# Optimization experiments

Hardware: AMD Instinct MI355X
Metric: run time of the kernel (lower is better)

## Reference

```python
import jax, jax.numpy as jnp
import numpy as np

EPS = float(np.finfo(np.float64).eps)  # np.finfo(float).eps as in torch combine


def setup_inputs() -> dict:
    key = jax.random.key(0)
    ks = jax.random.split(key, 4)
    B, E, D_in, D_h, D_out = 4096, 8, 768, 2048, 768
    return {
        "x": jax.random.normal(ks[0], (B, D_in), dtype=jnp.float32),
        "w_gate": jax.random.normal(ks[1], (D_in, E), dtype=jnp.float32) * 0.02,
        "W1": jax.random.normal(ks[2], (E, D_in, D_h), dtype=jnp.float32) * (1.0 / np.sqrt(D_in)),
        "b1": jnp.zeros((E, D_h), dtype=jnp.float32),
        "W2": jax.random.normal(ks[3], (E, D_h, D_out), dtype=jnp.float32) * (1.0 / np.sqrt(D_h)),
        "b2": jnp.zeros((E, D_out), dtype=jnp.float32),
        "k": 2,
    }


def _cv_squared(v):
    # torch .var() is unbiased (ddof=1)
    return jnp.var(v, ddof=1) / (jnp.mean(v) ** 2 + 1e-10)


def _top_k_gates(logits, k):
    B, E = logits.shape
    top_vals, top_idx = jax.lax.top_k(logits, k)        # [B, k]
    top_gates = jax.nn.softmax(top_vals, axis=1)        # softmax over the k kept logits
    gates = jnp.zeros((B, E), logits.dtype).at[jnp.arange(B)[:, None], top_idx].set(top_gates)
    return gates


def reference(x, w_gate, W1, b1, W2, b2, k):
    # --- gating (eval path: noiseless clean logits, softmax gating) ---
    logits = x @ w_gate                                  # [B, E]
    gates = _top_k_gates(logits, k)                      # [B, E], sparse (k nonzeros/row)
    # --- per-expert MLP: Linear -> gelu -> Linear -> log_softmax ---
    # Dense grouped compute over experts; gate==0 terms contribute nothing in combine.
    h = jax.nn.gelu(jnp.einsum('bi,eih->beh', x, W1) + b1[None])      # [B, E, Dh]
    lo = jax.nn.log_softmax(jnp.einsum('beh,eho->beo', h, W2) + b2[None], axis=-1)  # [B, E, Do]
    # --- combine: exp, weight by gates, scatter-add, eps-clamp, log ---
    combined = jnp.einsum('be,beo->bo', gates, jnp.exp(lo))           # [B, Do]
    y = jnp.log(jnp.where(combined == 0, EPS, combined))
    # --- load-balancing aux loss (eval: load = count of nonzero gates) ---
    importance = gates.sum(0)
    load = (gates > 0).sum(0).astype(jnp.float32)
    loss = 0.01 * (_cv_squared(importance) + _cv_squared(load))
    return y, loss
```

## Files before the change

kernel.cpp:

```cpp
#include <hip/hip_runtime.h>
#include <hip/hip_bf16.h>
#include <math.h>

typedef __hip_bfloat16 bf16;
typedef short v8s __attribute__((ext_vector_type(8)));
typedef float v4f __attribute__((ext_vector_type(4)));

#define B_TOK 4096
#define E_EXP 8
#define D_IN  768
#define D_H   2048
#define D_OUT 768
#define MAXT  72

__device__ __forceinline__ void gl_lds16(const bf16* g, bf16* l) {
  __builtin_amdgcn_global_load_lds(
      (const __attribute__((address_space(1))) unsigned int*)g,
      (__attribute__((address_space(3))) unsigned int*)l, 16, 0, 0);
}

__device__ __forceinline__ void transpose_tile64(
    const float* __restrict__ W, bf16* __restrict__ Wt,
    int K, int N, int e, int k0, int n0, int t, bf16 (*tile)[72]) {
  const int w = t >> 6, l = t & 63;
  const float* Wp = W + (size_t)e * K * N;
  #pragma unroll
  for (int p = 0; p < 4; ++p) {
    int k_loc = w * 16 + p * 4 + (l >> 4);
    int nn = (l & 15) * 4;
    float4 v = *(const float4*)(Wp + (size_t)(k0 + k_loc) * N + n0 + nn);
    float vv[4] = {v.x, v.y, v.z, v.w};
    #pragma unroll
    for (int i = 0; i < 4; ++i) {
      int n_loc = nn + i;
      int phys = (k_loc >> 3) ^ ((n_loc >> 2) & 7);
      tile[n_loc][phys * 8 + (k_loc & 7)] = __float2bfloat16(vv[i]);
    }
  }
  __syncthreads();
  bf16* Wtp = Wt + (size_t)e * N * K;
  const int nsub = l >> 2;
  #pragma unroll
  for (int p2 = 0; p2 < 2; ++p2) {
    int c = (l & 3) + p2 * 4;
    int n_loc = w * 16 + nsub;
    int phys = c ^ ((n_loc >> 2) & 7);
    v8s val = *(const v8s*)&tile[n_loc][phys * 8];
    *(v8s*)(Wtp + (size_t)(n0 + n_loc) * K + k0 + c * 8) = val;
  }
}

__global__ __launch_bounds__(256)
void prep_kernel(const float* __restrict__ x, const float* __restrict__ wg,
                 const float* __restrict__ W1, bf16* __restrict__ W1t,
                 bf16* __restrict__ xb, float* __restrict__ gates,
                 int* __restrict__ tidx) {
  __shared__ bf16 tile[64][72];
  const int b = blockIdx.x;
  const int t = threadIdx.x;
  if (b < 3072) {
    int e = b / 384, rem = b % 384;
    int kb = rem % 12, nb = rem / 12;
    transpose_tile64(W1, W1t, D_IN, D_H, e, kb * 64, nb * 64, t, tile);
  } else {
    int gt = (b - 3072) * 256 + t;
    int tok = gt >> 6, l = gt & 63;
    const float* xr = x + (size_t)tok * D_IN;
    bf16* xbr = xb + (size_t)tok * D_IN;
    float acc[8] = {0.f,0.f,0.f,0.f,0.f,0.f,0.f,0.f};
    #pragma unroll
    for (int i = 0; i < 3; ++i) {
      int k0 = i * 256 + l * 4;
      float4 v = *(const float4*)(xr + k0);
      union { bf16 h[4]; uint2 u; } pk;
      pk.h[0] = __float2bfloat16(v.x); pk.h[1] = __float2bfloat16(v.y);
      pk.h[2] = __float2bfloat16(v.z); pk.h[3] = __float2bfloat16(v.w);
      *(uint2*)(xbr + k0) = pk.u;
      float xv[4] = {v.x, v.y, v.z, v.w};
      #pragma unroll
      for (int j = 0; j < 4; ++j) {
        const float* wr = wg + (size_t)(k0 + j) * 8;
        float4 w0 = *(const float4*)wr;
        float4 w1 = *(const float4*)(wr + 4);
        acc[0] += xv[j] * w0.x; acc[1] += xv[j] * w0.y;
        acc[2] += xv[j] * w0.z; acc[3] += xv[j] * w0.w;
        acc[4] += xv[j] * w1.x; acc[5] += xv[j] * w1.y;
        acc[6] += xv[j] * w1.z; acc[7] += xv[j] * w1.w;
      }
    }
    #pragma unroll
    for (int d = 1; d < 64; d <<= 1)
      #pragma unroll
      for (int e2 = 0; e2 < 8; ++e2) acc[e2] += __shfl_xor(acc[e2], d);
    if (l == 0) {
      int i1 = 0; float v1 = acc[0];
      #pragma unroll
      for (int e2 = 1; e2 < 8; ++e2) if (acc[e2] > v1) { v1 = acc[e2]; i1 = e2; }
      int i2 = -1; float v2 = -1e30f;
      #pragma unroll
      for (int e2 = 0; e2 < 8; ++e2) if (e2 != i1 && acc[e2] > v2) { v2 = acc[e2]; i2 = e2; }
      float ex = __expf(v2 - v1);
      float g1 = 1.f / (1.f + ex), g2 = ex / (1.f + ex);
      gates[2 * tok] = g1; gates[2 * tok + 1] = g2;
      tidx[2 * tok] = i1;  tidx[2 * tok + 1] = i2;
    }
  }
}

__global__ void finalize_kernel(const int* __restrict__ tidx, const float* __restrict__ gates,
                                int* __restrict__ cnt_off, int* __restrict__ row_ids,
                                int* __restrict__ pos, int* __restrict__ tmap,
                                float* __restrict__ loss_out) {
  __shared__ int   hcnt[256][9];
  __shared__ float himp[256][9];
  __shared__ int   tot[8], off[8];
  __shared__ float itot[8];
  int t = threadIdx.x;
  #pragma unroll
  for (int e = 0; e < 8; ++e) { hcnt[t][e] = 0; himp[t][e] = 0.f; }
  __syncthreads();
  for (int i = 0; i < 32; ++i) {
    int idx = t * 32 + i;
    int e = tidx[idx];
    hcnt[t][e] += 1;
    himp[t][e] += gates[idx];
  }
  __syncthreads();
  if (t < 8) {
    int run = 0; float s = 0.f;
    for (int j = 0; j < 256; ++j) {
      int c = hcnt[j][t];
      hcnt[j][t] = run;
      run += c;
      s += himp[j][t];
    }
    tot[t] = run; itot[t] = s;
  }
  __syncthreads();
  if (t == 0) {
    int o = 0;
    float mi = 0.f, ml = 0.f;
    for (int e = 0; e < 8; ++e) {
      off[e] = o; o += tot[e];
      cnt_off[e] = tot[e]; cnt_off[8 + e] = off[e];
      mi += itot[e]; ml += (float)tot[e];
    }
    mi *= 0.125f; ml *= 0.125f;
    float vi = 0.f, vl = 0.f;
    for (int e = 0; e < 8; ++e) {
      float d = itot[e] - mi;        vi += d * d;
      float d2 = (float)tot[e] - ml; vl += d2 * d2;
    }
    vi /= 7.f; vl /= 7.f;
    *loss_out = 0.01f * (vi / (mi * mi + 1e-10f) + vl / (ml * ml + 1e-10f));
    int nt = 0;
    for (int e = 0; e < 8; ++e)
      for (int tt = 0; tt < (tot[e] + 127) >> 7; ++tt) {
        tmap[nt] = e; tmap[MAXT + nt] = tt; ++nt;
      }
    for (; nt < MAXT; ++nt) tmap[nt] = -1;
  }
  __syncthreads();
  for (int i = 0; i < 32; ++i) {
    int idx = t * 32 + i;
    int e = tidx[idx];
    int slot = off[e] + hcnt[t][e];
    hcnt[t][e] += 1;
    row_ids[slot] = idx >> 1;
    pos[idx] = slot;
  }
}

template<int KDIM, bool GATHER, bool GELU, bool DOTRANS>
__global__ __launch_bounds__(256, 2)
void gemm_bn256(const bf16* __restrict__ Ab, const bf16* __restrict__ Wt,
                const float* __restrict__ bias, bf16* __restrict__ Outb,
                const int* __restrict__ row_ids, const int* __restrict__ cnt_off,
                const int* __restrict__ tmap, const int N,
                const float* __restrict__ Wsrc, bf16* __restrict__ Wdst) {
  constexpr int BK = 32, BM = 128, BN = 256;
  constexpr int NK = KDIM / BK;
  static_assert(NK % 2 == 0 && NK >= 4, "NK even, >=4");
  __shared__ __align__(16) bf16 lds[2][(BM + BN) * BK];
  const int t = (int)threadIdx.x, w = t >> 6, l = t & 63;
  if (DOTRANS && blockIdx.y >= MAXT) {
    int tid = (blockIdx.y - MAXT) * gridDim.x + blockIdx.x;
    int e = tid / 96, r = tid % 96;
    int kb = r % 8, nb = r / 8;
    bf16 (*tile)[72] = (bf16(*)[72])&lds[0][0];
    #pragma unroll 1
    for (int sub = 0; sub < 4; ++sub) {
      transpose_tile64(Wsrc, Wdst, D_H, D_OUT, e, kb * 256 + sub * 64, nb * 64, t, tile);
      __syncthreads();
    }
    return;
  }
  const int ti = blockIdx.y;
  const int e = tmap[ti];
  if (e < 0) return;
  const int rowb = tmap[MAXT + ti];
  const int cnt = cnt_off[e];
  const int off = cnt_off[8 + e];
  const int colb = blockIdx.x;
  const int cs = (l & 3) ^ ((l >> 3) & 3);
  const bf16* gA[2];
  const bf16* gB[4];
  #pragma unroll
  for (int it = 0; it < 2; ++it) {
    int rt = (it * 4 + w) * 16 + (l >> 2);
    int r = rowb * BM + rt;
    int rc = r < cnt ? r : cnt - 1;
    long arow = GATHER ? (long)row_ids[off + rc] : (long)(off + rc);
    gA[it] = Ab + arow * (long)KDIM + cs * 8;
  }
  #pragma unroll
  for (int it = 0; it < 4; ++it) {
    int rt = (it * 4 + w) * 16 + (l >> 2);
    gB[it] = Wt + ((size_t)e * N + (size_t)colb * BN + rt) * KDIM + cs * 8;
  }
  v4f acc[4][8] = {};
  const int wm = w >> 1, wn = w & 1;

#define STAGE(b, k0) do {                                                   \
    _Pragma("unroll")                                                       \
    for (int it = 0; it < 2; ++it)                                          \
      gl_lds16(gA[it] + (k0), &lds[b][(it * 4 + w) * 512]);                 \
    _Pragma("unroll")                                                       \
    for (int it = 0; it < 4; ++it)                                          \
      gl_lds16(gB[it] + (k0), &lds[b][BM * BK + (it * 4 + w) * 512]);       \
  } while (0)

#define COMPUTE(b) do {                                                     \
    __builtin_amdgcn_s_setprio(1);                                          \
    v8s af[4], bfr[8];                                                      \
    const int p = (l >> 4) ^ ((l >> 1) & 3);                                \
    _Pragma("unroll")                                                       \
    for (int fm = 0; fm < 4; ++fm) {                                        \
      int row = wm * 64 + fm * 16 + (l & 15);                               \
      af[fm] = *(const v8s*)(&lds[b][0] + row * BK + p * 8);                \
    }                                                                       \
    _Pragma("unroll")                                                       \
    for (int fn = 0; fn < 8; ++fn) {                                        \
      int row = wn * 128 + fn * 16 + (l & 15);                              \
      bfr[fn] = *(const v8s*)(&lds[b][BM * BK] + row * BK + p * 8);         \
    }                                                                       \
    _Pragma("unroll")                                                       \
    for (int fm = 0; fm < 4; ++fm)                                          \
      _Pragma("unroll")                                                     \
      for (int fn = 0; fn < 8; ++fn)                                        \
        acc[fm][fn] = __builtin_amdgcn_mfma_f32_16x16x32_bf16(af[fm], bfr[fn], acc[fm][fn], 0, 0, 0); \
    __builtin_amdgcn_s_setprio(0);                                          \
  } while (0)

#define SB    __builtin_amdgcn_sched_barrier(0)
#define BARR  __builtin_amdgcn_s_barrier()
#define WAIT6 asm volatile("s_waitcnt vmcnt(6)" ::: "memory")
#define WAITZ asm volatile("s_waitcnt vmcnt(0)" ::: "memory")

  STAGE(0, 0);
  #pragma unroll 1
  for (int ks = 0; ks < NK - 2; ks += 2) {
    STAGE(1, (ks + 1) * BK);
    WAIT6; SB; BARR; SB;
    COMPUTE(0);
    BARR; SB;
    STAGE(0, (ks + 2) * BK);
    WAIT6; SB; BARR; SB;
    COMPUTE(1);
    BARR; SB;
  }
  STAGE(1, (NK - 1) * BK);
  WAIT6; SB; BARR; SB;
  COMPUTE(0);
  WAITZ; SB; BARR; SB;
  COMPUTE(1);
  BARR; SB;
#undef STAGE
#undef COMPUTE
#undef WAIT6
#undef WAITZ

  float* eps = (float*)(&lds[0][0]) + w * (16 * 132);
  const float* bpp = bias + (size_t)e * N + (size_t)colb * BN + wn * 128;
  float bv[2][8];
  #pragma unroll
  for (int pp = 0; pp < 2; ++pp)
    #pragma unroll
    for (int jj = 0; jj < 8; ++jj) bv[pp][jj] = bpp[pp * 64 + (l & 7) * 8 + jj];
  #pragma unroll
  for (int fm = 0; fm < 4; ++fm) {
    #pragma unroll
    for (int fn = 0; fn < 8; ++fn)
      #pragma unroll
      for (int q = 0; q < 4; ++q)
        eps[((l >> 4) * 4 + q) * 132 + fn * 16 + (l & 15)] = acc[fm][fn][q];
    #pragma unroll
    for (int half = 0; half < 2; ++half) {
      int row = (l >> 3) + 8 * half;
      int r = rowb * BM + wm * 64 + fm * 16 + row;
      if (r < cnt) {
        #pragma unroll
        for (int pp = 0; pp < 2; ++pp) {
          const float* rp = eps + row * 132 + pp * 64 + (l & 7) * 8;
          union { bf16 h[8]; uint4 u; } pk;
          #pragma unroll
          for (int jj = 0; jj < 8; ++jj) {
            float v = rp[jj] + bv[pp][jj];
            if (GELU) {
              float u = 0.7978845608028654f * (v + 0.044715f * v * v * v);
              float th = 1.f - 2.f / (__expf(2.f * u) + 1.f);
              v = 0.5f * v * (1.f + th);
            }
            pk.h[jj] = __float2bfloat16(v);
          }
          *(uint4*)(Outb + (size_t)(off + r) * N + (size_t)colb * BN
                    + wn * 128 + pp * 64 + (l & 7) * 8) = pk.u;
        }
      }
    }
  }
#undef SB
#undef BARR
}

template<int KDIM, bool GELU>
__global__ __launch_bounds__(256, 4)
void gemm_bk32(const bf16* __restrict__ Ab, const bf16* __restrict__ Wt,
               const float* __restrict__ bias, bf16* __restrict__ Outb,
               const int* __restrict__ cnt_off, const int* __restrict__ tmap,
               const int N) {
  constexpr int BK = 32, BM = 128, BN = 128;
  constexpr int NK = KDIM / BK;
  static_assert(NK % 2 == 0 && NK >= 4, "NK even, >=4");
  __shared__ __align__(16) bf16 lds[2][(BM + BN) * BK];
  const int t = (int)threadIdx.x, w = t >> 6, l = t & 63;
  const int ti = blockIdx.y;
  const int e = tmap[ti];
  if (e < 0) return;
  const int rowb = tmap[MAXT + ti];
  const int cnt = cnt_off[e];
  const int off = cnt_off[8 + e];
  const int colb = blockIdx.x;
  const int cs = (l & 3) ^ ((l >> 3) & 3);
  const bf16* gA[2];
  const bf16* gB[2];
  #pragma unroll
  for (int it = 0; it < 2; ++it) {
    int rt = (it * 4 + w) * 16 + (l >> 2);
    int r = rowb * BM + rt;
    int rc = r < cnt ? r : cnt - 1;
    gA[it] = Ab + (long)(off + rc) * KDIM + cs * 8;
    gB[it] = Wt + ((size_t)e * N + (size_t)colb * BN + rt) * KDIM + cs * 8;
  }
  v4f acc[4][4] = {};
  const int wm = w >> 1, wn = w & 1;

#define STAGE(b, k0) do {                                                   \
    _Pragma("unroll")                                                       \
    for (int it = 0; it < 2; ++it)                                          \
      gl_lds16(gA[it] + (k0), &lds[b][(it * 4 + w) * 512]);                 \
    _Pragma("unroll")                                                       \
    for (int it = 0; it < 2; ++it)                                          \
      gl_lds16(gB[it] + (k0), &lds[b][BM * BK + (it * 4 + w) * 512]);       \
  } while (0)

#define COMPUTE(b) do {                                                     \
    __builtin_amdgcn_s_setprio(1);                                          \
    v8s af[4], bfr[4];                                                      \
    const int p = (l >> 4) ^ ((l >> 1) & 3);                                \
    _Pragma("unroll")                                                       \
    for (int fm = 0; fm < 4; ++fm) {                                        \
      int row = wm * 64 + fm * 16 + (l & 15);                               \
      af[fm] = *(const v8s*)(&lds[b][0] + row * BK + p * 8);                \
    }                                                                       \
    _Pragma("unroll")                                                       \
    for (int fn = 0; fn < 4; ++fn) {                                        \
      int row = wn * 64 + fn * 16 + (l & 15);                               \
      bfr[fn] = *(const v8s*)(&lds[b][BM * BK] + row * BK + p * 8);         \
    }                                                                       \
    _Pragma("unroll")                                                       \
    for (int fm = 0; fm < 4; ++fm)                                          \
      _Pragma("unroll")                                                     \
      for (int fn = 0; fn < 4; ++fn)                                        \
        acc[fm][fn] = __builtin_amdgcn_mfma_f32_16x16x32_bf16(af[fm], bfr[fn], acc[fm][fn], 0, 0, 0); \
    __builtin_amdgcn_s_setprio(0);                                          \
  } while (0)

#define SB    __builtin_amdgcn_sched_barrier(0)
#define BARR  __builtin_amdgcn_s_barrier()
#define WAIT4 asm volatile("s_waitcnt vmcnt(4)" ::: "memory")
#define WAITZ asm volatile("s_waitcnt vmcnt(0)" ::: "memory")

  STAGE(0, 0);
  #pragma unroll 1
  for (int ks = 0; ks < NK - 2; ks += 2) {
    STAGE(1, (ks + 1) * BK);
    WAIT4; SB; BARR; SB;
    COMPUTE(0);
    BARR; SB;
    STAGE(0, (ks + 2) * BK);
    WAIT4; SB; BARR; SB;
    COMPUTE(1);
    BARR; SB;
  }
  STAGE(1, (NK - 1) * BK);
  WAIT4; SB; BARR; SB;
  COMPUTE(0);
  WAITZ; SB; BARR; SB;
  COMPUTE(1);
  BARR; SB;
#undef STAGE
#undef COMPUTE
#undef WAIT4
#undef WAITZ

  float* eps = (float*)(&lds[0][0]) + w * (16 * 68);
  const float* bp = bias + (size_t)e * N + (size_t)colb * BN + wn * 64 + (l & 7) * 8;
  float bv[8];
  #pragma unroll
  for (int jj = 0; jj < 8; ++jj) bv[jj] = bp[jj];
  #pragma unroll
  for (int fm = 0; fm < 4; ++fm) {
    #pragma unroll
    for (int fn = 0; fn < 4; ++fn)
      #pragma unroll
      for (int q = 0; q < 4; ++q)
        eps[((l >> 4) * 4 + q) * 68 + fn * 16 + (l & 15)] = acc[fm][fn][q];
    #pragma unroll
    for (int half = 0; half < 2; ++half) {
      int row = (l >> 3) + 8 * half;
      int r = rowb * BM + wm * 64 + fm * 16 + row;
      if (r < cnt) {
        const float* rp = eps + row * 68 + (l & 7) * 8;
        union { bf16 h[8]; uint4 u; } pk;
        #pragma unroll
        for (int jj = 0; jj < 8; ++jj) {
          float v = rp[jj] + bv[jj];
          if (GELU) {
            float u = 0.7978845608028654f * (v + 0.044715f * v * v * v);
            float th = 1.f - 2.f / (__expf(2.f * u) + 1.f);
            v = 0.5f * v * (1.f + th);
          }
          pk.h[jj] = __float2bfloat16(v);
        }
        *(uint4*)(Outb + (size_t)(off + r) * N + (size_t)colb * BN + wn * 64 + (l & 7) * 8) = pk.u;
      }
    }
  }
#undef SB
#undef BARR
}

__global__ void combine_kernel(const bf16* __restrict__ z, const float* __restrict__ gates,
                               const int* __restrict__ pos, float* __restrict__ y) {
  int gt = blockIdx.x * 256 + threadIdx.x;
  int tok = gt >> 6, l = gt & 63;
  if (tok >= B_TOK) return;
  const ushort4* z1 = (const ushort4*)(z + (size_t)pos[2 * tok] * D_OUT);
  const ushort4* z2 = (const ushort4*)(z + (size_t)pos[2 * tok + 1] * D_OUT);
  float g1 = gates[2 * tok], g2 = gates[2 * tok + 1];
  float a[12], b[12];
  float m1 = -1e30f, m2 = -1e30f;
  #pragma unroll
  for (int i = 0; i < 3; ++i) {
    ushort4 u1 = z1[l + i * 64];
    ushort4 u2 = z2[l + i * 64];
    unsigned s1v[4] = {u1.x, u1.y, u1.z, u1.w};
    unsigned s2v[4] = {u2.x, u2.y, u2.z, u2.w};
    #pragma unroll
    for (int j = 0; j < 4; ++j) {
      union { unsigned u; float f; } c1, c2;
      c1.u = s1v[j] << 16; c2.u = s2v[j] << 16;
      a[i * 4 + j] = c1.f; b[i * 4 + j] = c2.f;
      m1 = fmaxf(m1, c1.f); m2 = fmaxf(m2, c2.f);
    }
  }
  #pragma unroll
  for (int d = 1; d < 64; d <<= 1) {
    m1 = fmaxf(m1, __shfl_xor(m1, d));
    m2 = fmaxf(m2, __shfl_xor(m2, d));
  }
  float s1 = 0.f, s2 = 0.f;
  #pragma unroll
  for (int i = 0; i < 12; ++i) { s1 += __expf(a[i] - m1); s2 += __expf(b[i] - m2); }
  #pragma unroll
  for (int d = 1; d < 64; d <<= 1) { s1 += __shfl_xor(s1, d); s2 += __shfl_xor(s2, d); }
  float c1 = g1 / s1, c2 = g2 / s2;
  float4* yo = (float4*)(y + (size_t)tok * D_OUT);
  #pragma unroll
  for (int i = 0; i < 3; ++i) {
    float4 o;
    float* op = (float*)&o;
    #pragma unroll
    for (int j = 0; j < 4; ++j) {
      float cmb = c1 * __expf(a[i * 4 + j] - m1) + c2 * __expf(b[i * 4 + j] - m2);
      op[j] = logf(cmb == 0.f ? 2.2204460492503131e-16f : cmb);
    }
    yo[l + i * 64] = o;
  }
}

extern "C" void kernel_launch(void* const* d_in, const int* in_sizes, int n_in,
                              void* d_out, int out_size, void* d_ws, size_t ws_size,
                              hipStream_t stream) {
  const float* x  = (const float*)d_in[0];
  const float* wg = (const float*)d_in[1];
  const float* W1 = (const float*)d_in[2];
  const float* b1 = (const float*)d_in[3];
  const float* W2 = (const float*)d_in[4];
  const float* b2 = (const float*)d_in[5];
  float* out = (float*)d_out;

  char* ws = (char*)d_ws;
  int*   cnt_off = (int*)(ws + 0);
  float* gates   = (float*)(ws + 256);
  int*   tidx    = (int*)(ws + 256 + 32768);
  int*   pos     = (int*)(ws + 256 + 65536);
  int*   row_ids = (int*)(ws + 256 + 98304);
  int*   tmap    = (int*)(ws + 256 + 131072);
  const size_t base = 262144;
  bf16* x_bf = (bf16*)(ws + base);
  bf16* W1t  = (bf16*)(ws + base + 6291456);
  bf16* W2t  = (bf16*)(ws + base + 31457280);
  bf16* h_bf = (bf16*)(ws + base + 56623104);
  bf16* z_bf = (bf16*)(ws + base);

  prep_kernel<<<dim3(4096), 256, 0, stream>>>(x, wg, W1, W1t, x_bf, gates, tidx);
  finalize_kernel<<<dim3(1), 256, 0, stream>>>(tidx, gates, cnt_off, row_ids, pos, tmap,
                                               out + (size_t)B_TOK * D_OUT);
  gemm_bn256<D_IN, true, true, true><<<dim3(D_H / 256, MAXT + 96), 256, 0, stream>>>(
      x_bf, W1t, b1, h_bf, row_ids, cnt_off, tmap, D_H, W2, W2t);
  gemm_bk32<D_H, false><<<dim3(D_OUT / 128, MAXT), 256, 0, stream>>>(
      h_bf, W2t, b2, z_bf, cnt_off, tmap, D_OUT);
  combine_kernel<<<dim3(1024), 256, 0, stream>>>(z_bf, gates, pos, out);
}
```

Baseline: 162.9 us.

## Shrink first GEMM tile to BN=128; load second GEMM weights directly to registers

The first expert GEMM (fused with the gather, GELU and W2 transpose) now uses 128x128 tiles with higher occupancy instead of 128x256 tiles. The transpose work is spread over the new grid shape. The second GEMM gets a new kernel that stages only the activation tile through LDS and loads weight fragments straight from global memory into registers, double-buffered alongside the LDS stage. This aims to cut LDS traffic and footprint and raise occupancy, at the risk of less coalesced global reads of weights and less weight reuse across waves.

```diff
diff --git a/kernel.cpp b/kernel.cpp
--- a/kernel.cpp
+++ b/kernel.cpp
@@ -172,13 +172,13 @@
 }
 
 template<int KDIM, bool GATHER, bool GELU, bool DOTRANS>
-__global__ __launch_bounds__(256, 2)
-void gemm_bn256(const bf16* __restrict__ Ab, const bf16* __restrict__ Wt,
-                const float* __restrict__ bias, bf16* __restrict__ Outb,
-                const int* __restrict__ row_ids, const int* __restrict__ cnt_off,
-                const int* __restrict__ tmap, const int N,
-                const float* __restrict__ Wsrc, bf16* __restrict__ Wdst) {
-  constexpr int BK = 32, BM = 128, BN = 256;
+__global__ __launch_bounds__(256, 4)
+void gemm_bk32(const bf16* __restrict__ Ab, const bf16* __restrict__ Wt,
+               const float* __restrict__ bias, bf16* __restrict__ Outb,
+               const int* __restrict__ row_ids, const int* __restrict__ cnt_off,
+               const int* __restrict__ tmap, const int N,
+               const float* __restrict__ Wsrc, bf16* __restrict__ Wdst) {
+  constexpr int BK = 32, BM = 128, BN = 128;
   constexpr int NK = KDIM / BK;
   static_assert(NK % 2 == 0 && NK >= 4, "NK even, >=4");
   __shared__ __align__(16) bf16 lds[2][(BM + BN) * BK];
@@ -204,7 +204,7 @@
   const int colb = blockIdx.x;
   const int cs = (l & 3) ^ ((l >> 3) & 3);
   const bf16* gA[2];
-  const bf16* gB[4];
+  const bf16* gB[2];
   #pragma unroll
   for (int it = 0; it < 2; ++it) {
     int rt = (it * 4 + w) * 16 + (l >> 2);
@@ -212,144 +212,6 @@
     int rc = r < cnt ? r : cnt - 1;
     long arow = GATHER ? (long)row_ids[off + rc] : (long)(off + rc);
     gA[it] = Ab + arow * (long)KDIM + cs * 8;
-  }
-  #pragma unroll
-  for (int it = 0; it < 4; ++it) {
-    int rt = (it * 4 + w) * 16 + (l >> 2);
-    gB[it] = Wt + ((size_t)e * N + (size_t)colb * BN + rt) * KDIM + cs * 8;
-  }
-  v4f acc[4][8] = {};
-  const int wm = w >> 1, wn = w & 1;
-
-#define STAGE(b, k0) do {                                                   \
-    _Pragma("unroll")                                                       \
-    for (int it = 0; it < 2; ++it)                                          \
-      gl_lds16(gA[it] + (k0), &lds[b][(it * 4 + w) * 512]);                 \
-    _Pragma("unroll")                                                       \
-    for (int it = 0; it < 4; ++it)                                          \
-      gl_lds16(gB[it] + (k0), &lds[b][BM * BK + (it * 4 + w) * 512]);       \
-  } while (0)
-
-#define COMPUTE(b) do {                                                     \
-    __builtin_amdgcn_s_setprio(1);                                          \
-    v8s af[4], bfr[8];                                                      \
-    const int p = (l >> 4) ^ ((l >> 1) & 3);                                \
-    _Pragma("unroll")                                                       \
-    for (int fm = 0; fm < 4; ++fm) {                                        \
-      int row = wm * 64 + fm * 16 + (l & 15);                               \
-      af[fm] = *(const v8s*)(&lds[b][0] + row * BK + p * 8);                \
-    }                                                                       \
-    _Pragma("unroll")                                                       \
-    for (int fn = 0; fn < 8; ++fn) {                                        \
-      int row = wn * 128 + fn * 16 + (l & 15);                              \
-      bfr[fn] = *(const v8s*)(&lds[b][BM * BK] + row * BK + p * 8);         \
-    }                                                                       \
-    _Pragma("unroll")                                                       \
-    for (int fm = 0; fm < 4; ++fm)                                          \
-      _Pragma("unroll")                                                     \
-      for (int fn = 0; fn < 8; ++fn)                                        \
-        acc[fm][fn] = __builtin_amdgcn_mfma_f32_16x16x32_bf16(af[fm], bfr[fn], acc[fm][fn], 0, 0, 0); \
-    __builtin_amdgcn_s_setprio(0);                                          \
-  } while (0)
-
-#define SB    __builtin_amdgcn_sched_barrier(0)
-#define BARR  __builtin_amdgcn_s_barrier()
-#define WAIT6 asm volatile("s_waitcnt vmcnt(6)" ::: "memory")
-#define WAITZ asm volatile("s_waitcnt vmcnt(0)" ::: "memory")
-
-  STAGE(0, 0);
-  #pragma unroll 1
-  for (int ks = 0; ks < NK - 2; ks += 2) {
-    STAGE(1, (ks + 1) * BK);
-    WAIT6; SB; BARR; SB;
-    COMPUTE(0);
-    BARR; SB;
-    STAGE(0, (ks + 2) * BK);
-    WAIT6; SB; BARR; SB;
-    COMPUTE(1);
-    BARR; SB;
-  }
-  STAGE(1, (NK - 1) * BK);
-  WAIT6; SB; BARR; SB;
-  COMPUTE(0);
-  WAITZ; SB; BARR; SB;
-  COMPUTE(1);
-  BARR; SB;
-#undef STAGE
-#undef COMPUTE
-#undef WAIT6
-#undef WAITZ
-
-  float* eps = (float*)(&lds[0][0]) + w * (16 * 132);
-  const float* bpp = bias + (size_t)e * N + (size_t)colb * BN + wn * 128;
-  float bv[2][8];
-  #pragma unroll
-  for (int pp = 0; pp < 2; ++pp)
-    #pragma unroll
-    for (int jj = 0; jj < 8; ++jj) bv[pp][jj] = bpp[pp * 64 + (l & 7) * 8 + jj];
-  #pragma unroll
-  for (int fm = 0; fm < 4; ++fm) {
-    #pragma unroll
-    for (int fn = 0; fn < 8; ++fn)
-      #pragma unroll
-      for (int q = 0; q < 4; ++q)
-        eps[((l >> 4) * 4 + q) * 132 + fn * 16 + (l & 15)] = acc[fm][fn][q];
-    #pragma unroll
-    for (int half = 0; half < 2; ++half) {
-      int row = (l >> 3) + 8 * half;
-      int r = rowb * BM + wm * 64 + fm * 16 + row;
-      if (r < cnt) {
-        #pragma unroll
-        for (int pp = 0; pp < 2; ++pp) {
-          const float* rp = eps + row * 132 + pp * 64 + (l & 7) * 8;
-          union { bf16 h[8]; uint4 u; } pk;
-          #pragma unroll
-          for (int jj = 0; jj < 8; ++jj) {
-            float v = rp[jj] + bv[pp][jj];
-            if (GELU) {
-              float u = 0.7978845608028654f * (v + 0.044715f * v * v * v);
-              float th = 1.f - 2.f / (__expf(2.f * u) + 1.f);
-              v = 0.5f * v * (1.f + th);
-            }
-            pk.h[jj] = __float2bfloat16(v);
-          }
-          *(uint4*)(Outb + (size_t)(off + r) * N + (size_t)colb * BN
-                    + wn * 128 + pp * 64 + (l & 7) * 8) = pk.u;
-        }
-      }
-    }
-  }
-#undef SB
-#undef BARR
-}
-
-template<int KDIM, bool GELU>
-__global__ __launch_bounds__(256, 4)
-void gemm_bk32(const bf16* __restrict__ Ab, const bf16* __restrict__ Wt,
-               const float* __restrict__ bias, bf16* __restrict__ Outb,
-               const int* __restrict__ cnt_off, const int* __restrict__ tmap,
-               const int N) {
-  constexpr int BK = 32, BM = 128, BN = 128;
-  constexpr int NK = KDIM / BK;
-  static_assert(NK % 2 == 0 && NK >= 4, "NK even, >=4");
-  __shared__ __align__(16) bf16 lds[2][(BM + BN) * BK];
-  const int t = (int)threadIdx.x, w = t >> 6, l = t & 63;
-  const int ti = blockIdx.y;
-  const int e = tmap[ti];
-  if (e < 0) return;
-  const int rowb = tmap[MAXT + ti];
-  const int cnt = cnt_off[e];
-  const int off = cnt_off[8 + e];
-  const int colb = blockIdx.x;
-  const int cs = (l & 3) ^ ((l >> 3) & 3);
-  const bf16* gA[2];
-  const bf16* gB[2];
-  #pragma unroll
-  for (int it = 0; it < 2; ++it) {
-    int rt = (it * 4 + w) * 16 + (l >> 2);
-    int r = rowb * BM + rt;
-    int rc = r < cnt ? r : cnt - 1;
-    gA[it] = Ab + (long)(off + rc) * KDIM + cs * 8;
     gB[it] = Wt + ((size_t)e * N + (size_t)colb * BN + rt) * KDIM + cs * 8;
   }
   v4f acc[4][4] = {};
@@ -451,6 +313,141 @@
 #undef BARR
 }
 
+template<int KDIM, bool GELU>
+__global__ __launch_bounds__(256, 3)
+void gemm_directb(const bf16* __restrict__ Ab, const bf16* __restrict__ Wt,
+                  const float* __restrict__ bias, bf16* __restrict__ Outb,
+                  const int* __restrict__ cnt_off, const int* __restrict__ tmap,
+                  const int N) {
+  constexpr int BK = 32, BM = 128;
+  constexpr int NK = KDIM / BK;
+  static_assert(NK % 2 == 0 && NK >= 4, "NK even, >=4");
+  __shared__ __align__(16) bf16 lds[9216];
+  const int t = (int)threadIdx.x, w = t >> 6, l = t & 63;
+  const int ti = blockIdx.y;
+  const int e = tmap[ti];
+  if (e < 0) return;
+  const int rowb = tmap[MAXT + ti];
+  const int cnt = cnt_off[e];
+  const int off = cnt_off[8 + e];
+  const int colb = blockIdx.x;
+  const int cs = (l & 3) ^ ((l >> 3) & 3);
+  const int wm = w >> 1, wn = w & 1;
+  const bf16* gA[2];
+  #pragma unroll
+  for (int it = 0; it < 2; ++it) {
+    int rt = (it * 4 + w) * 16 + (l >> 2);
+    int r = rowb * BM + rt;
+    int rc = r < cnt ? r : cnt - 1;
+    gA[it] = Ab + (long)(off + rc) * KDIM + cs * 8;
+  }
+  const bf16* gBp[4];
+  #pragma unroll
+  for (int fn = 0; fn < 4; ++fn) {
+    int n = colb * 128 + wn * 64 + fn * 16 + (l & 15);
+    gBp[fn] = Wt + ((size_t)e * N + n) * KDIM + (l >> 4) * 8;
+  }
+  v4f acc[4][4] = {};
+  v8s bA[4], bB[4];
+
+#define STAGEA(boff, k0) do {                                               \
+    _Pragma("unroll")                                                       \
+    for (int it = 0; it < 2; ++it)                                          \
+      gl_lds16(gA[it] + (k0), lds + (boff) + (it * 4 + w) * 512);           \
+  } while (0)
+#define LOADB(dst, k0) do {                                                 \
+    _Pragma("unroll")                                                       \
+    for (int fn = 0; fn < 4; ++fn)                                          \
+      dst[fn] = *(const v8s*)(gBp[fn] + (k0));                              \
+  } while (0)
+#define COMPUTE(boff, bset) do {                                            \
+    __builtin_amdgcn_s_setprio(1);                                          \
+    v8s af[4];                                                              \
+    const int p = (l >> 4) ^ ((l >> 1) & 3);                                \
+    _Pragma("unroll")                                                       \
+    for (int fm = 0; fm < 4; ++fm) {                                        \
+      int row = wm * 64 + fm * 16 + (l & 15);                               \
+      af[fm] = *(const v8s*)(lds + (boff) + row * BK + p * 8);              \
+    }                                                                       \
+    _Pragma("unroll")                                                       \
+    for (int fm = 0; fm < 4; ++fm)                                          \
+      _Pragma("unroll")                                                     \
+      for (int fn = 0; fn < 4; ++fn)                                        \
+        acc[fm][fn] = __builtin_amdgcn_mfma_f32_16x16x32_bf16(af[fm], bset[fn], acc[fm][fn], 0, 0, 0); \
+    __builtin_amdgcn_s_setprio(0);                                          \
+  } while (0)
+
+#define SB    __builtin_amdgcn_sched_barrier(0)
+#define BARR  __builtin_amdgcn_s_barrier()
+#define WAIT6 asm volatile("s_waitcnt vmcnt(6)" ::: "memory")
+#define WAITZ asm volatile("s_waitcnt vmcnt(0)" ::: "memory")
+
+  STAGEA(0, 0);
+  LOADB(bA, 0);
+  #pragma unroll 1
+  for (int ks = 0; ks < NK - 2; ks += 2) {
+    STAGEA(4608, (ks + 1) * BK);
+    LOADB(bB, (ks + 1) * BK);
+    WAIT6; SB; BARR; SB;
+    COMPUTE(0, bA);
+    BARR; SB;
+    STAGEA(0, (ks + 2) * BK);
+    LOADB(bA, (ks + 2) * BK);
+    WAIT6; SB; BARR; SB;
+    COMPUTE(4608, bB);
+    BARR; SB;
+  }
+  STAGEA(4608, (NK - 1) * BK);
+  LOADB(bB, (NK - 1) * BK);
+  WAIT6; SB; BARR; SB;
+  COMPUTE(0, bA);
+  WAITZ; SB; BARR; SB;
+  COMPUTE(4608, bB);
+  BARR; SB;
+#undef STAGEA
+#undef LOADB
+#undef COMPUTE
+#undef WAIT6
+#undef WAITZ
+
+  float* eps = (float*)lds + w * (16 * 68);
+  const float* bp = bias + (size_t)e * N + (size_t)colb * 128 + wn * 64 + (l & 7) * 8;
+  float bv[8];
+  #pragma unroll
+  for (int jj = 0; jj < 8; ++jj) bv[jj] = bp[jj];
+  #pragma unroll
+  for (int fm = 0; fm < 4; ++fm) {
+    #pragma unroll
+    for (int fn = 0; fn < 4; ++fn)
+      #pragma unroll
+      for (int q = 0; q < 4; ++q)
+        eps[((l >> 4) * 4 + q) * 68 + fn * 16 + (l & 15)] = acc[fm][fn][q];
+    #pragma unroll
+    for (int half = 0; half < 2; ++half) {
+      int row = (l >> 3) + 8 * half;
+      int r = rowb * BM + wm * 64 + fm * 16 + row;
+      if (r < cnt) {
+        const float* rp = eps + row * 68 + (l & 7) * 8;
+        union { bf16 h[8]; uint4 u; } pk;
+        #pragma unroll
+        for (int jj = 0; jj < 8; ++jj) {
+          float v = rp[jj] + bv[jj];
+          if (GELU) {
+            float u = 0.7978845608028654f * (v + 0.044715f * v * v * v);
+            float th = 1.f - 2.f / (__expf(2.f * u) + 1.f);
+            v = 0.5f * v * (1.f + th);
+          }
+          pk.h[jj] = __float2bfloat16(v);
+        }
+        *(uint4*)(Outb + (size_t)(off + r) * N + (size_t)colb * 128 + wn * 64 + (l & 7) * 8) = pk.u;
+      }
+    }
+    BARR;
+  }
+#undef SB
+#undef BARR
+}
+
 __global__ void combine_kernel(const bf16* __restrict__ z, const float* __restrict__ gates,
                                const int* __restrict__ pos, float* __restrict__ y) {
   int gt = blockIdx.x * 256 + threadIdx.x;
@@ -528,9 +525,9 @@
   prep_kernel<<<dim3(4096), 256, 0, stream>>>(x, wg, W1, W1t, x_bf, gates, tidx);
   finalize_kernel<<<dim3(1), 256, 0, stream>>>(tidx, gates, cnt_off, row_ids, pos, tmap,
                                                out + (size_t)B_TOK * D_OUT);
-  gemm_bn256<D_IN, true, true, true><<<dim3(D_H / 256, MAXT + 96), 256, 0, stream>>>(
+  gemm_bk32<D_IN, true, true, true><<<dim3(D_H / 128, MAXT + 48), 256, 0, stream>>>(
       x_bf, W1t, b1, h_bf, row_ids, cnt_off, tmap, D_H, W2, W2t);
-  gemm_bk32<D_H, false><<<dim3(D_OUT / 128, MAXT), 256, 0, stream>>>(
+  gemm_directb<D_H, false><<<dim3(D_OUT / 128, MAXT), 256, 0, stream>>>(
       h_bf, W2t, b2, z_bf, cnt_off, tmap, D_OUT);
   combine_kernel<<<dim3(1024), 256, 0, stream>>>(z_bf, gates, pos, out);
 }
```

After: 180.8 us. 1.11x slower.
